# Kernel optimization log

Hardware: AMD Instinct MI355X
Metric: run time of the kernel (lower is better)

Reference implementation:

```python
import jax, jax.numpy as jnp
import numpy as np

DIM = 1024
N_HEADS = 16
DIM_FF = 4096
EPS = 1e-12


def layer_norm(x, gamma, beta):
    u = jnp.mean(x, axis=-1, keepdims=True)
    s = jnp.mean((x - u) ** 2, axis=-1, keepdims=True)
    return gamma * ((x - u) / jnp.sqrt(s + EPS)) + beta


def setup_inputs() -> dict:
    key = jax.random.key(0)
    ks = jax.random.split(key, 12)
    B, S, D, F = 2, 2048, DIM, DIM_FF
    init = lambda k, shape: (jax.random.normal(k, shape, dtype=jnp.float32) * 0.02)
    return {
        "x": jax.random.normal(ks[0], (B, S, D), dtype=jnp.float32),
        "mask": jnp.ones((B, S), dtype=jnp.int32),
        "wq": init(ks[1], (D, D)), "bq": jnp.zeros((D,), jnp.float32),
        "wk": init(ks[2], (D, D)), "bk": jnp.zeros((D,), jnp.float32),
        "wv": init(ks[3], (D, D)), "bv": jnp.zeros((D,), jnp.float32),
        "wo": init(ks[4], (D, D)), "bo": jnp.zeros((D,), jnp.float32),
        "g1": jnp.ones((D,), jnp.float32), "b1": jnp.zeros((D,), jnp.float32),
        "w1": init(ks[5], (D, F)), "bf1": jnp.zeros((F,), jnp.float32),
        "w2": init(ks[6], (F, D)), "bf2": jnp.zeros((D,), jnp.float32),
        "g2": jnp.ones((D,), jnp.float32), "b2": jnp.zeros((D,), jnp.float32),
    }


def reference(x, mask, wq, bq, wk, bk, wv, bv, wo, bo, g1, b1, w1, bf1, w2, bf2, g2, b2):
    B, S, D = x.shape
    H = N_HEADS
    W = D // H
    # QKV projections -> (B, H, S, W)
    def heads(y):
        return y.reshape(B, S, H, W).transpose(0, 2, 1, 3)
    q = heads(x @ wq + bq)
    k = heads(x @ wk + bk)
    v = heads(x @ wv + bv)
    # scaled dot-product attention with additive mask (exact module math)
    scores = jnp.einsum('bhsw,bhtw->bhst', q, k) / np.sqrt(W).astype(np.float32)
    m = mask.astype(jnp.float32)[:, None, None, :]  # (B,1,1,S)
    scores = scores - 10000.0 * (1.0 - m)
    attn = jax.nn.softmax(scores, axis=-1)
    h = jnp.einsum('bhst,bhtw->bhsw', attn, v).transpose(0, 2, 1, 3).reshape(B, S, D)
    # residual + LN1
    h = layer_norm(x + (h @ wo + bo), g1, b1)
    # position-wise FFN with exact-erf GELU, residual + LN2
    ff = jax.nn.gelu(h @ w1 + bf1, approximate=False) @ w2 + bf2
    return layer_norm(h + ff, g2, b2)
```

## Files before the change

### kernel.cpp

```cpp
#include <hip/hip_runtime.h>
#include <cstdint>
#include <cstddef>

using u16 = unsigned short;
using u32 = unsigned int;

typedef __bf16 bf16x8 __attribute__((ext_vector_type(8)));
typedef float f32x4 __attribute__((ext_vector_type(4)));

static constexpr int Bb = 2, S = 2048, D = 1024, H = 16, W = 64, F = 4096;
static constexpr int M = Bb * S;

__device__ __forceinline__ float bf2f(u16 u) {
  union { u32 i; float f; } c; c.i = ((u32)u) << 16; return c.f;
}
__device__ __forceinline__ u16 f2bf(float f) {
  union { float f; u32 i; } c; c.f = f;
  u32 i = c.i;
  u32 r = (i + 0x7fffu + ((i >> 16) & 1u)) >> 16;
  return (u16)r;
}
__device__ __forceinline__ u16 f2bf_cvt(float f) {
  __bf16 b = (__bf16)f;
  union { __bf16 b; u16 u; } c; c.b = b; return c.u;
}
__device__ __forceinline__ __bf16 u2b(u16 x) {
  union { u16 u; __bf16 b; } c; c.u = x; return c.b;
}
__device__ __forceinline__ void stv(float* p, size_t i, float v) { p[i] = v; }
__device__ __forceinline__ void stv(u16* p, size_t i, float v)   { p[i] = f2bf(v); }
__device__ __forceinline__ float ldv(const float* p, size_t i) { return p[i]; }
__device__ __forceinline__ float ldv(const u16* p, size_t i)   { return bf2f(p[i]); }

__device__ __forceinline__ void async_cp16(const u16* g, u16* l) {
  __builtin_amdgcn_global_load_lds(
      (const __attribute__((address_space(1))) void*)g,
      (__attribute__((address_space(3))) void*)l, 16, 0, 0);
}

__global__ __launch_bounds__(256) void conv_x_kernel(
    const float* __restrict__ src, u16* __restrict__ dst)
{
  int i = (blockIdx.x * 256 + threadIdx.x) * 4;
  float4 v = *(const float4*)(src + i);
  u16 r[4] = { f2bf(v.x), f2bf(v.y), f2bf(v.z), f2bf(v.w) };
  *(uint2*)(dst + i) = *(const uint2*)r;
}

__global__ __launch_bounds__(256) void transpose_w_kernel(
    const float* __restrict__ src, u16* __restrict__ dst, int K, int N)
{
  __shared__ __align__(16) u16 T[64][72];
  const int tid = threadIdx.x;
  const int n0 = blockIdx.x * 64, k0 = blockIdx.y * 64;
#pragma unroll
  for (int t = 0; t < 4; t++) {
    int idx = tid + t * 256;
    int r = idx >> 4, c4 = (idx & 15) * 4;
    float4 v = *(const float4*)(src + (size_t)(k0 + r) * N + n0 + c4);
    T[c4 + 0][r] = f2bf(v.x); T[c4 + 1][r] = f2bf(v.y);
    T[c4 + 2][r] = f2bf(v.z); T[c4 + 3][r] = f2bf(v.w);
  }
  __syncthreads();
#pragma unroll
  for (int t = 0; t < 2; t++) {
    int idx = tid + t * 256;
    int r = idx >> 3, c8 = (idx & 7) * 8;
    *(uint4*)(dst + (size_t)(n0 + r) * K + k0 + c8) = *(const uint4*)(&T[r][c8]);
  }
}

template<int EPI, typename TC>
__global__ __launch_bounds__(256) void gemm_bt(
    const u16* __restrict__ A, const u16* __restrict__ BT,
    const float* __restrict__ bias, TC* __restrict__ C,
    int N, int K, float scale)
{
  __shared__ __align__(16) u16 As[128 * 32];
  __shared__ __align__(16) u16 Bs[128 * 32];
  const int tid = threadIdx.x;
  const int wave = tid >> 6, lane = tid & 63;
  const int quad = lane >> 4, l16 = lane & 15;
  const int m0 = blockIdx.y * 128, n0 = blockIdx.x * 128;
  const int wm = (wave >> 1) * 64, wn = (wave & 1) * 64;
  const int srow = lane >> 2;
  const int skoff = (lane & 3) * 8;

  f32x4 acc[4][4] = {};

  for (int k0 = 0; k0 < K; k0 += 32) {
#pragma unroll
    for (int t = 0; t < 2; t++) {
      int slot = wave * 2 + t;
      int row = slot * 16 + srow;
      const u16* ga = A  + (size_t)(m0 + row) * K + k0 + skoff;
      const u16* gb = BT + (size_t)(n0 + row) * K + k0 + skoff;
      async_cp16(ga, As + slot * 512);
      async_cp16(gb, Bs + slot * 512);
    }
    __syncthreads();

    bf16x8 af[4], bfv[4];
#pragma unroll
    for (int i = 0; i < 4; i++)
      af[i] = *(const bf16x8*)(As + (wm + i * 16 + l16) * 32 + quad * 8);
#pragma unroll
    for (int j = 0; j < 4; j++)
      bfv[j] = *(const bf16x8*)(Bs + (wn + j * 16 + l16) * 32 + quad * 8);
#pragma unroll
    for (int i = 0; i < 4; i++)
#pragma unroll
      for (int j = 0; j < 4; j++)
        acc[i][j] = __builtin_amdgcn_mfma_f32_16x16x32_bf16(af[i], bfv[j], acc[i][j], 0, 0, 0);
    __syncthreads();
  }

#pragma unroll
  for (int i = 0; i < 4; i++) {
#pragma unroll
    for (int j = 0; j < 4; j++) {
#pragma unroll
      for (int r = 0; r < 4; r++) {
        int row = m0 + wm + i * 16 + quad * 4 + r;
        int col = n0 + wn + j * 16 + l16;
        float val = acc[i][j][r] + bias[col];
        if (EPI == 1) {
          val = 0.5f * val * (1.0f + erff(val * 0.70710678118654752f));
        }
        if (EPI == 2) {
          int sel = col >> 10, c = col & 1023;
          if (sel == 0) val *= scale;
          int bb = row >> 11, ss = row & 2047;
          int hh = c >> 6,  ww = c & 63;
          u16* dst = (u16*)C + (size_t)sel * M * D;
          dst[(((size_t)(bb * H + hh) * S) + ss) * W + ww] = f2bf(val);
        } else {
          stv(C, (size_t)row * N + col, val);
        }
      }
    }
  }
}

template<typename TC>
__global__ __launch_bounds__(256) void gemm_bt_n64(
    const u16* __restrict__ A, const u16* __restrict__ BT,
    const float* __restrict__ bias, TC* __restrict__ C,
    int N, int K)
{
  __shared__ __align__(16) u16 As[128 * 32];
  __shared__ __align__(16) u16 Bs[64 * 32];
  const int tid = threadIdx.x;
  const int wave = tid >> 6, lane = tid & 63;
  const int quad = lane >> 4, l16 = lane & 15;
  const int m0 = blockIdx.y * 128, n0 = blockIdx.x * 64;
  const int wm = (wave >> 1) * 64, wn = (wave & 1) * 32;
  const int srow = lane >> 2;
  const int skoff = (lane & 3) * 8;

  f32x4 acc[4][2] = {};

  for (int k0 = 0; k0 < K; k0 += 32) {
#pragma unroll
    for (int t = 0; t < 2; t++) {
      int slot = wave * 2 + t;
      int row = slot * 16 + srow;
      async_cp16(A + (size_t)(m0 + row) * K + k0 + skoff, As + slot * 512);
    }
    {
      int row = wave * 16 + srow;
      async_cp16(BT + (size_t)(n0 + row) * K + k0 + skoff, Bs + wave * 512);
    }
    __syncthreads();

    bf16x8 af[4], bfv[2];
#pragma unroll
    for (int i = 0; i < 4; i++)
      af[i] = *(const bf16x8*)(As + (wm + i * 16 + l16) * 32 + quad * 8);
#pragma unroll
    for (int j = 0; j < 2; j++)
      bfv[j] = *(const bf16x8*)(Bs + (wn + j * 16 + l16) * 32 + quad * 8);
#pragma unroll
    for (int i = 0; i < 4; i++)
#pragma unroll
      for (int j = 0; j < 2; j++)
        acc[i][j] = __builtin_amdgcn_mfma_f32_16x16x32_bf16(af[i], bfv[j], acc[i][j], 0, 0, 0);
    __syncthreads();
  }

#pragma unroll
  for (int i = 0; i < 4; i++) {
#pragma unroll
    for (int j = 0; j < 2; j++) {
#pragma unroll
      for (int r = 0; r < 4; r++) {
        int row = m0 + wm + i * 16 + quad * 4 + r;
        int col = n0 + wn + j * 16 + l16;
        stv(C, (size_t)row * N + col, acc[i][j][r] + bias[col]);
      }
    }
  }
}

__global__ __launch_bounds__(256) void transpose_v_kernel(
    const u16* __restrict__ v, u16* __restrict__ vt)
{
  __shared__ __align__(16) u16 T[64][72];
  const int bh = blockIdx.y, k0 = blockIdx.x * 64, tid = threadIdx.x;
#pragma unroll
  for (int it = 0; it < 2; it++) {
    int vv = tid + it * 256;
    int key = vv >> 3, w0 = (vv & 7) * 8;
    union { uint4 q; u16 e[8]; } u;
    u.q = *(const uint4*)(v + ((size_t)bh * S + k0 + key) * W + w0);
#pragma unroll
    for (int j = 0; j < 8; j++) T[w0 + j][key] = u.e[j];
  }
  __syncthreads();
#pragma unroll
  for (int it = 0; it < 2; it++) {
    int vv = tid + it * 256;
    int w = vv >> 3, koff = (vv & 7) * 8;
    *(uint4*)(vt + ((size_t)bh * W + w) * S + k0 + koff) = *(const uint4*)(&T[w][koff]);
  }
}

__global__ __launch_bounds__(256) void fattn_kernel(
    const u16* __restrict__ q, const u16* __restrict__ k,
    const u16* __restrict__ vt, const int* __restrict__ mask,
    u16* __restrict__ out)
{
  __shared__ __align__(16) u16 QP[64][72];
  __shared__ __align__(16) u16 Kl[64][72];
  __shared__ __align__(16) u16 Vl[64][72];
  __shared__ float msk[64];

  const int tid = threadIdx.x, wave = tid >> 6, lane = tid & 63;
  const int quad = lane >> 4, l16 = lane & 15;
  const int bh = blockIdx.y, b = bh >> 4, h = bh & 15;
  const int q0 = blockIdx.x * 64;
  const int w16 = wave * 16;

#pragma unroll
  for (int it = 0; it < 2; it++) {
    int vv = tid + it * 256;
    int r = vv >> 3, c0 = (vv & 7) * 8;
    *(uint4*)(&QP[r][c0]) = *(const uint4*)(q + ((size_t)bh * S + q0 + r) * W + c0);
  }
  __syncthreads();
  bf16x8 aq[2];
#pragma unroll
  for (int kc = 0; kc < 2; kc++)
    aq[kc] = *(const bf16x8*)(&QP[w16 + l16][kc * 32 + quad * 8]);

  bf16x8 ones;
  {
    u16 ov = (l16 == 0) ? (u16)0x3F80 : (u16)0;
#pragma unroll
    for (int j = 0; j < 8; j++) ones[j] = u2b(ov);
  }

  float m_run = -1e30f;
  f32x4 o_acc[4] = {};
  f32x4 l_acc = {};

  for (int kt = 0; kt < S / 64; kt++) {
    __syncthreads();
#pragma unroll
    for (int it = 0; it < 2; it++) {
      int vv = tid + it * 256;
      int r = vv >> 3, c0 = (vv & 7) * 8;
      *(uint4*)(&Kl[r][c0]) = *(const uint4*)(k  + ((size_t)bh * S + kt * 64 + r) * W + c0);
      *(uint4*)(&Vl[r][c0]) = *(const uint4*)(vt + ((size_t)bh * W + r) * S + kt * 64 + c0);
    }
    if (tid < 64) msk[tid] = -10000.0f * (1.0f - (float)mask[b * S + kt * 64 + tid]);
    __syncthreads();

    f32x4 sc[4] = {};
#pragma unroll
    for (int tn = 0; tn < 4; tn++) {
#pragma unroll
      for (int kc = 0; kc < 2; kc++) {
        bf16x8 bk = *(const bf16x8*)(&Kl[tn * 16 + l16][kc * 32 + quad * 8]);
        sc[tn] = __builtin_amdgcn_mfma_f32_16x16x32_bf16(aq[kc], bk, sc[tn], 0, 0, 0);
      }
    }
    float lmax = -1e30f;
#pragma unroll
    for (int tn = 0; tn < 4; tn++) {
      float mm = msk[tn * 16 + l16];
#pragma unroll
      for (int r = 0; r < 4; r++) {
        sc[tn][r] += mm;
        lmax = fmaxf(lmax, sc[tn][r]);
      }
    }
#pragma unroll
    for (int d = 1; d < 64; d <<= 1) lmax = fmaxf(lmax, __shfl_xor(lmax, d));
    float mnew = fmaxf(m_run, lmax);
    float alpha = __expf(m_run - mnew);
    m_run = mnew;

#pragma unroll
    for (int tn = 0; tn < 4; tn++) {
#pragma unroll
      for (int r = 0; r < 4; r++) {
        float pv = __expf(sc[tn][r] - mnew);
        QP[w16 + quad * 4 + r][tn * 16 + l16] = f2bf_cvt(pv);
      }
    }
    if (alpha < 1.0f) {
#pragma unroll
      for (int tn = 0; tn < 4; tn++)
#pragma unroll
        for (int r = 0; r < 4; r++) o_acc[tn][r] *= alpha;
#pragma unroll
      for (int r = 0; r < 4; r++) l_acc[r] *= alpha;
    }

#pragma unroll
    for (int kc = 0; kc < 2; kc++) {
      bf16x8 ap = *(const bf16x8*)(&QP[w16 + l16][kc * 32 + quad * 8]);
#pragma unroll
      for (int tn = 0; tn < 4; tn++) {
        bf16x8 bv = *(const bf16x8*)(&Vl[tn * 16 + l16][kc * 32 + quad * 8]);
        o_acc[tn] = __builtin_amdgcn_mfma_f32_16x16x32_bf16(ap, bv, o_acc[tn], 0, 0, 0);
      }
      l_acc = __builtin_amdgcn_mfma_f32_16x16x32_bf16(ap, ones, l_acc, 0, 0, 0);
    }
  }

#pragma unroll
  for (int r = 0; r < 4; r++) {
    float lsum = __shfl(l_acc[r], lane & 0x30);
    float inv = 1.0f / lsum;
    int sg = q0 + w16 + quad * 4 + r;
#pragma unroll
    for (int tn = 0; tn < 4; tn++) {
      out[((size_t)b * S + sg) * D + h * W + tn * 16 + l16] = f2bf_cvt(o_acc[tn][r] * inv);
    }
  }
}

template<typename TA, typename TR, typename TO>
__global__ __launch_bounds__(256) void ln_res_kernel(
    const TA* __restrict__ a, const TR* __restrict__ r,
    const float* __restrict__ g, const float* __restrict__ be,
    TO* __restrict__ out)
{
  const int row = blockIdx.x;
  const int tid = threadIdx.x;
  __shared__ float red[256];
  const TA* ap = a + (size_t)row * D;
  const TR* rp = r + (size_t)row * D;
  float hv[4];
  float lsum = 0.f;
#pragma unroll
  for (int c = 0; c < 4; c++) {
    int d = tid + c * 256;
    hv[c] = ldv(ap, d) + ldv(rp, d);
    lsum += hv[c];
  }
  red[tid] = lsum; __syncthreads();
  for (int st = 128; st > 0; st >>= 1) { if (tid < st) red[tid] += red[tid + st]; __syncthreads(); }
  float mean = red[0] * (1.0f / D);
  __syncthreads();
  float lv = 0.f;
#pragma unroll
  for (int c = 0; c < 4; c++) { float dd = hv[c] - mean; lv += dd * dd; }
  red[tid] = lv; __syncthreads();
  for (int st = 128; st > 0; st >>= 1) { if (tid < st) red[tid] += red[tid + st]; __syncthreads(); }
  float varr = red[0] * (1.0f / D);
  float inv = rsqrtf(varr + 1e-12f);
#pragma unroll
  for (int c = 0; c < 4; c++) {
    int d = tid + c * 256;
    stv(out, (size_t)row * D + d, g[d] * ((hv[c] - mean) * inv) + be[d]);
  }
}

extern "C" void kernel_launch(void* const* d_in, const int* in_sizes, int n_in,
                              void* d_out, int out_size, void* d_ws, size_t ws_size,
                              hipStream_t stream)
{
  const float* x  = (const float*)d_in[0];
  const int* mask = (const int*)d_in[1];
  const float* wq = (const float*)d_in[2];  const float* bq  = (const float*)d_in[3];
  const float* wk = (const float*)d_in[4];  const float* bk  = (const float*)d_in[5];
  const float* wv = (const float*)d_in[6];  const float* bv  = (const float*)d_in[7];
  const float* wo = (const float*)d_in[8];  const float* bo  = (const float*)d_in[9];
  const float* g1 = (const float*)d_in[10]; const float* b1  = (const float*)d_in[11];
  const float* w1 = (const float*)d_in[12]; const float* bf1 = (const float*)d_in[13];
  const float* w2 = (const float*)d_in[14]; const float* bf2 = (const float*)d_in[15];
  const float* g2 = (const float*)d_in[16]; const float* b2  = (const float*)d_in[17];

  char* ws = (char*)d_ws;
  const size_t MB = 1024 * 1024;
  u16* wqkvT = (u16*)(ws + 0 * MB);
  u16* woT   = (u16*)(ws + 6 * MB);
  u16* w1T   = (u16*)(ws + 0 * MB);
  u16* w2T   = (u16*)(ws + 0 * MB);
  u16* xb    = (u16*)(ws + 8 * MB);
  u16* vt    = (u16*)(ws + 8 * MB);
  u16* q     = (u16*)(ws + 16 * MB);
  u16* proj  = (u16*)(ws + 16 * MB);
  u16* kb    = (u16*)(ws + 24 * MB);
  u16* vb    = (u16*)(ws + 32 * MB);
  u16* attn  = (u16*)(ws + 32 * MB);
  u16* ff1   = (u16*)(ws + 8 * MB);
  float* bqkv = (float*)(ws + 40 * MB);
  u16* h1    = (u16*)(ws + 40 * MB);
  float* out = (float*)d_out;

  dim3 blk(256);

  conv_x_kernel<<<dim3(M * D / 1024), blk, 0, stream>>>(x, xb);
  transpose_w_kernel<<<dim3(16, 16), blk, 0, stream>>>(wq, wqkvT,            D, D);
  transpose_w_kernel<<<dim3(16, 16), blk, 0, stream>>>(wk, wqkvT + 1024*1024, D, D);
  transpose_w_kernel<<<dim3(16, 16), blk, 0, stream>>>(wv, wqkvT + 2048*1024, D, D);
  transpose_w_kernel<<<dim3(16, 16), blk, 0, stream>>>(wo, woT,              D, D);
  hipMemcpyAsync(bqkv,        bq, D * sizeof(float), hipMemcpyDeviceToDevice, stream);
  hipMemcpyAsync(bqkv + 1024, bk, D * sizeof(float), hipMemcpyDeviceToDevice, stream);
  hipMemcpyAsync(bqkv + 2048, bv, D * sizeof(float), hipMemcpyDeviceToDevice, stream);

  gemm_bt<2, u16><<<dim3(3072 / 128, M / 128), blk, 0, stream>>>(
      xb, wqkvT, bqkv, q, 3072, D, 0.125f);

  transpose_v_kernel<<<dim3(S / 64, Bb * H), blk, 0, stream>>>(vb, vt);
  fattn_kernel<<<dim3(S / 64, Bb * H), blk, 0, stream>>>(q, kb, vt, mask, attn);

  gemm_bt_n64<u16><<<dim3(D / 64, M / 128), blk, 0, stream>>>(
      attn, woT, bo, proj, D, D);
  ln_res_kernel<float, u16, u16><<<dim3(M), blk, 0, stream>>>(x, proj, g1, b1, h1);

  transpose_w_kernel<<<dim3(F / 64, D / 64), blk, 0, stream>>>(w1, w1T, D, F);
  gemm_bt<1, u16><<<dim3(F / 128, M / 128), blk, 0, stream>>>(
      h1, w1T, bf1, ff1, F, D, 1.0f);

  transpose_w_kernel<<<dim3(D / 64, F / 64), blk, 0, stream>>>(w2, w2T, F, D);
  gemm_bt_n64<float><<<dim3(D / 64, M / 128), blk, 0, stream>>>(
      ff1, w2T, bf2, out, D, F);
  ln_res_kernel<u16, float, float><<<dim3(M), blk, 0, stream>>>(h1, out, g2, b2, out);
}
```

Baseline: 460.8 us.

## Deepen GEMM K-step, prefetch attention K/V into registers, warp-per-row layernorm

Both GEMM kernels now load two 32-wide K slabs per barrier pair (K step 64), which halves the number of syncthreads per tile and doubles the LDS footprint. The flash-attention kernel prefetches the next K/V tile and mask into registers while the current tile is computed, so global load latency overlaps with MFMA work. The layernorm kernel processes one row per wavefront using shuffle reductions instead of a 256-thread shared-memory tree, launching four rows per block. The gains depend on latency hiding versus the extra register and LDS pressure, which could lower occupancy.

```diff
diff --git a/kernel.cpp b/kernel.cpp
--- a/kernel.cpp
+++ b/kernel.cpp
@@ -76,8 +76,8 @@
     const float* __restrict__ bias, TC* __restrict__ C,
     int N, int K, float scale)
 {
-  __shared__ __align__(16) u16 As[128 * 32];
-  __shared__ __align__(16) u16 Bs[128 * 32];
+  __shared__ __align__(16) u16 As[2][128 * 32];
+  __shared__ __align__(16) u16 Bs[2][128 * 32];
   const int tid = threadIdx.x;
   const int wave = tid >> 6, lane = tid & 63;
   const int quad = lane >> 4, l16 = lane & 15;
@@ -88,30 +88,36 @@
 
   f32x4 acc[4][4] = {};
 
-  for (int k0 = 0; k0 < K; k0 += 32) {
-#pragma unroll
-    for (int t = 0; t < 2; t++) {
-      int slot = wave * 2 + t;
-      int row = slot * 16 + srow;
-      const u16* ga = A  + (size_t)(m0 + row) * K + k0 + skoff;
-      const u16* gb = BT + (size_t)(n0 + row) * K + k0 + skoff;
-      async_cp16(ga, As + slot * 512);
-      async_cp16(gb, Bs + slot * 512);
-    }
-    __syncthreads();
-
-    bf16x8 af[4], bfv[4];
-#pragma unroll
-    for (int i = 0; i < 4; i++)
-      af[i] = *(const bf16x8*)(As + (wm + i * 16 + l16) * 32 + quad * 8);
-#pragma unroll
-    for (int j = 0; j < 4; j++)
-      bfv[j] = *(const bf16x8*)(Bs + (wn + j * 16 + l16) * 32 + quad * 8);
-#pragma unroll
-    for (int i = 0; i < 4; i++)
+  for (int k0 = 0; k0 < K; k0 += 64) {
+#pragma unroll
+    for (int h = 0; h < 2; h++) {
+#pragma unroll
+      for (int t = 0; t < 2; t++) {
+        int slot = wave * 2 + t;
+        int row = slot * 16 + srow;
+        const u16* ga = A  + (size_t)(m0 + row) * K + k0 + h * 32 + skoff;
+        const u16* gb = BT + (size_t)(n0 + row) * K + k0 + h * 32 + skoff;
+        async_cp16(ga, As[h] + slot * 512);
+        async_cp16(gb, Bs[h] + slot * 512);
+      }
+    }
+    __syncthreads();
+
+#pragma unroll
+    for (int h = 0; h < 2; h++) {
+      bf16x8 af[4], bfv[4];
+#pragma unroll
+      for (int i = 0; i < 4; i++)
+        af[i] = *(const bf16x8*)(As[h] + (wm + i * 16 + l16) * 32 + quad * 8);
 #pragma unroll
       for (int j = 0; j < 4; j++)
-        acc[i][j] = __builtin_amdgcn_mfma_f32_16x16x32_bf16(af[i], bfv[j], acc[i][j], 0, 0, 0);
+        bfv[j] = *(const bf16x8*)(Bs[h] + (wn + j * 16 + l16) * 32 + quad * 8);
+#pragma unroll
+      for (int i = 0; i < 4; i++)
+#pragma unroll
+        for (int j = 0; j < 4; j++)
+          acc[i][j] = __builtin_amdgcn_mfma_f32_16x16x32_bf16(af[i], bfv[j], acc[i][j], 0, 0, 0);
+    }
     __syncthreads();
   }
 
@@ -148,8 +154,8 @@
     const float* __restrict__ bias, TC* __restrict__ C,
     int N, int K)
 {
-  __shared__ __align__(16) u16 As[128 * 32];
-  __shared__ __align__(16) u16 Bs[64 * 32];
+  __shared__ __align__(16) u16 As[2][128 * 32];
+  __shared__ __align__(16) u16 Bs[2][64 * 32];
   const int tid = threadIdx.x;
   const int wave = tid >> 6, lane = tid & 63;
   const int quad = lane >> 4, l16 = lane & 15;
@@ -160,31 +166,35 @@
 
   f32x4 acc[4][2] = {};
 
-  for (int k0 = 0; k0 < K; k0 += 32) {
-#pragma unroll
-    for (int t = 0; t < 2; t++) {
-      int slot = wave * 2 + t;
-      int row = slot * 16 + srow;
-      async_cp16(A + (size_t)(m0 + row) * K + k0 + skoff, As + slot * 512);
-    }
-    {
+  for (int k0 = 0; k0 < K; k0 += 64) {
+#pragma unroll
+    for (int h = 0; h < 2; h++) {
+#pragma unroll
+      for (int t = 0; t < 2; t++) {
+        int slot = wave * 2 + t;
+        int row = slot * 16 + srow;
+        async_cp16(A + (size_t)(m0 + row) * K + k0 + h * 32 + skoff, As[h] + slot * 512);
+      }
       int row = wave * 16 + srow;
-      async_cp16(BT + (size_t)(n0 + row) * K + k0 + skoff, Bs + wave * 512);
-    }
-    __syncthreads();
-
-    bf16x8 af[4], bfv[2];
-#pragma unroll
-    for (int i = 0; i < 4; i++)
-      af[i] = *(const bf16x8*)(As + (wm + i * 16 + l16) * 32 + quad * 8);
-#pragma unroll
-    for (int j = 0; j < 2; j++)
-      bfv[j] = *(const bf16x8*)(Bs + (wn + j * 16 + l16) * 32 + quad * 8);
-#pragma unroll
-    for (int i = 0; i < 4; i++)
+      async_cp16(BT + (size_t)(n0 + row) * K + k0 + h * 32 + skoff, Bs[h] + wave * 512);
+    }
+    __syncthreads();
+
+#pragma unroll
+    for (int h = 0; h < 2; h++) {
+      bf16x8 af[4], bfv[2];
+#pragma unroll
+      for (int i = 0; i < 4; i++)
+        af[i] = *(const bf16x8*)(As[h] + (wm + i * 16 + l16) * 32 + quad * 8);
 #pragma unroll
       for (int j = 0; j < 2; j++)
-        acc[i][j] = __builtin_amdgcn_mfma_f32_16x16x32_bf16(af[i], bfv[j], acc[i][j], 0, 0, 0);
+        bfv[j] = *(const bf16x8*)(Bs[h] + (wn + j * 16 + l16) * 32 + quad * 8);
+#pragma unroll
+      for (int i = 0; i < 4; i++)
+#pragma unroll
+        for (int j = 0; j < 2; j++)
+          acc[i][j] = __builtin_amdgcn_mfma_f32_16x16x32_bf16(af[i], bfv[j], acc[i][j], 0, 0, 0);
+    }
     __syncthreads();
   }
 
@@ -240,6 +250,8 @@
   const int bh = blockIdx.y, b = bh >> 4, h = bh & 15;
   const int q0 = blockIdx.x * 64;
   const int w16 = wave * 16;
+  const int sr = tid >> 3, sc0 = (tid & 7) * 8;
+  const int sr2 = (tid + 256) >> 3, sc2 = ((tid + 256) & 7) * 8;
 
 #pragma unroll
   for (int it = 0; it < 2; it++) {
@@ -264,17 +276,31 @@
   f32x4 o_acc[4] = {};
   f32x4 l_acc = {};
 
+  uint4 kr0, kr1, vr0, vr1;
+  int mv = 0;
+  kr0 = *(const uint4*)(k  + ((size_t)bh * S + sr ) * W + sc0);
+  kr1 = *(const uint4*)(k  + ((size_t)bh * S + sr2) * W + sc2);
+  vr0 = *(const uint4*)(vt + ((size_t)bh * W + sr ) * S + sc0);
+  vr1 = *(const uint4*)(vt + ((size_t)bh * W + sr2) * S + sc2);
+  if (tid < 64) mv = mask[b * S + tid];
+
   for (int kt = 0; kt < S / 64; kt++) {
     __syncthreads();
-#pragma unroll
-    for (int it = 0; it < 2; it++) {
-      int vv = tid + it * 256;
-      int r = vv >> 3, c0 = (vv & 7) * 8;
-      *(uint4*)(&Kl[r][c0]) = *(const uint4*)(k  + ((size_t)bh * S + kt * 64 + r) * W + c0);
-      *(uint4*)(&Vl[r][c0]) = *(const uint4*)(vt + ((size_t)bh * W + r) * S + kt * 64 + c0);
-    }
-    if (tid < 64) msk[tid] = -10000.0f * (1.0f - (float)mask[b * S + kt * 64 + tid]);
-    __syncthreads();
+    *(uint4*)(&Kl[sr ][sc0]) = kr0;
+    *(uint4*)(&Kl[sr2][sc2]) = kr1;
+    *(uint4*)(&Vl[sr ][sc0]) = vr0;
+    *(uint4*)(&Vl[sr2][sc2]) = vr1;
+    if (tid < 64) msk[tid] = -10000.0f * (1.0f - (float)mv);
+    __syncthreads();
+
+    if (kt + 1 < S / 64) {
+      int kn = (kt + 1) * 64;
+      kr0 = *(const uint4*)(k  + ((size_t)bh * S + kn + sr ) * W + sc0);
+      kr1 = *(const uint4*)(k  + ((size_t)bh * S + kn + sr2) * W + sc2);
+      vr0 = *(const uint4*)(vt + ((size_t)bh * W + sr ) * S + kn + sc0);
+      vr1 = *(const uint4*)(vt + ((size_t)bh * W + sr2) * S + kn + sc2);
+      if (tid < 64) mv = mask[b * S + kn + tid];
+    }
 
     f32x4 sc[4] = {};
 #pragma unroll
@@ -348,33 +374,30 @@
     const float* __restrict__ g, const float* __restrict__ be,
     TO* __restrict__ out)
 {
-  const int row = blockIdx.x;
-  const int tid = threadIdx.x;
-  __shared__ float red[256];
+  const int tid = threadIdx.x, lane = tid & 63;
+  const int row = blockIdx.x * 4 + (tid >> 6);
   const TA* ap = a + (size_t)row * D;
   const TR* rp = r + (size_t)row * D;
-  float hv[4];
-  float lsum = 0.f;
-#pragma unroll
-  for (int c = 0; c < 4; c++) {
-    int d = tid + c * 256;
+  float hv[16];
+  float s = 0.f;
+#pragma unroll
+  for (int c = 0; c < 16; c++) {
+    int d = c * 64 + lane;
     hv[c] = ldv(ap, d) + ldv(rp, d);
-    lsum += hv[c];
-  }
-  red[tid] = lsum; __syncthreads();
-  for (int st = 128; st > 0; st >>= 1) { if (tid < st) red[tid] += red[tid + st]; __syncthreads(); }
-  float mean = red[0] * (1.0f / D);
-  __syncthreads();
-  float lv = 0.f;
-#pragma unroll
-  for (int c = 0; c < 4; c++) { float dd = hv[c] - mean; lv += dd * dd; }
-  red[tid] = lv; __syncthreads();
-  for (int st = 128; st > 0; st >>= 1) { if (tid < st) red[tid] += red[tid + st]; __syncthreads(); }
-  float varr = red[0] * (1.0f / D);
-  float inv = rsqrtf(varr + 1e-12f);
-#pragma unroll
-  for (int c = 0; c < 4; c++) {
-    int d = tid + c * 256;
+    s += hv[c];
+  }
+#pragma unroll
+  for (int d = 1; d < 64; d <<= 1) s += __shfl_xor(s, d);
+  float mean = s * (1.0f / D);
+  float v = 0.f;
+#pragma unroll
+  for (int c = 0; c < 16; c++) { float t = hv[c] - mean; v += t * t; }
+#pragma unroll
+  for (int d = 1; d < 64; d <<= 1) v += __shfl_xor(v, d);
+  float inv = rsqrtf(v * (1.0f / D) + 1e-12f);
+#pragma unroll
+  for (int c = 0; c < 16; c++) {
+    int d = c * 64 + lane;
     stv(out, (size_t)row * D + d, g[d] * ((hv[c] - mean) * inv) + be[d]);
   }
 }
@@ -431,7 +454,7 @@
 
   gemm_bt_n64<u16><<<dim3(D / 64, M / 128), blk, 0, stream>>>(
       attn, woT, bo, proj, D, D);
-  ln_res_kernel<float, u16, u16><<<dim3(M), blk, 0, stream>>>(x, proj, g1, b1, h1);
+  ln_res_kernel<float, u16, u16><<<dim3(M / 4), blk, 0, stream>>>(x, proj, g1, b1, h1);
 
   transpose_w_kernel<<<dim3(F / 64, D / 64), blk, 0, stream>>>(w1, w1T, D, F);
   gemm_bt<1, u16><<<dim3(F / 128, M / 128), blk, 0, stream>>>(
@@ -440,5 +463,5 @@
   transpose_w_kernel<<<dim3(D / 64, F / 64), blk, 0, stream>>>(w2, w2T, F, D);
   gemm_bt_n64<float><<<dim3(D / 64, M / 128), blk, 0, stream>>>(
       ff1, w2T, bf2, out, D, F);
-  ln_res_kernel<u16, float, float><<<dim3(M), blk, 0, stream>>>(h1, out, g2, b2, out);
-}
+  ln_res_kernel<u16, float, float><<<dim3(M / 4), blk, 0, stream>>>(h1, out, g2, b2, out);
+}
```

New measurement: 451.8 us. Within noise of the previous version (-1.9%).
